# Kernel optimization log

Hardware: AMD Instinct MI355X
Metric: run time of the kernel (lower is better)

Reference implementation:

```python
import jax, jax.numpy as jnp
import numpy as np

NEARZERO = 1e-5
# Parameter bounds in dict order: BETA, FC, K0, K1, K2, LP, PERC, UZL, TT, CFMAX, CFR, CWH
BOUNDS = np.array([[1.0, 6.0], [50.0, 1000.0], [0.05, 0.9], [0.01, 0.5],
                   [0.001, 0.2], [0.2, 1.0], [0.0, 10.0], [0.0, 100.0],
                   [-2.5, 2.5], [0.5, 10.0], [0.0, 0.1], [0.0, 0.2]],
                  dtype=np.float32)


def setup_inputs() -> dict:
    key = jax.random.key(0)
    k1, k2, k3, k4 = jax.random.split(key, 4)
    T, G, nmul = 730, 4000, 8
    prcp = jax.random.uniform(k1, (T, G), dtype=jnp.float32) * 10.0   # mm/day, >= 0
    tmean = jax.random.normal(k2, (T, G), dtype=jnp.float32) * 10.0   # deg C
    pet = jax.random.uniform(k3, (T, G), dtype=jnp.float32) * 5.0     # mm/day, >= 0
    x_hydro_model = jnp.stack([prcp, tmean, pet], axis=-1)            # [T, G, 3]
    params_raw = jax.random.uniform(k4, (1, G, 12, nmul), dtype=jnp.float32)  # in [0,1)
    return {"x_hydro_model": x_hydro_model, "params_raw": params_raw}


def _hbv_forward(x_hydro_model, params_raw):
    G = x_hydro_model.shape[1]
    nmul = params_raw.shape[-1]
    b = jnp.asarray(BOUNDS)
    # change_param_range: param * (ub - lb) + lb, static slice at static_idx=-1
    p = params_raw[-1] * (b[:, 1] - b[:, 0])[None, :, None] + b[:, 0][None, :, None]  # [G,12,nmul]
    (BETA, FC, K0, K1, K2, LP, PERCc, UZL, TT, CFMAX, CFR, CWH) = [p[:, i, :] for i in range(12)]

    Pm = x_hydro_model[:, :, 0][:, :, None]    # [T, G, 1] broadcasts over nmul
    Tm = x_hydro_model[:, :, 1][:, :, None]
    PETm = x_hydro_model[:, :, 2][:, :, None]

    init = jnp.full((G, nmul), 0.001, dtype=jnp.float32)
    carry0 = (init, init, init, init, init)  # SNOWPACK, MELTWATER, SM, SUZ, SLZ

    def step(carry, inputs):
        SNOWPACK, MELTWATER, SM, SUZ, SLZ = carry
        PRECIP, Tt, PETt = inputs  # each [G, 1]
        is_rain = (Tt >= TT).astype(jnp.float32)
        RAIN = PRECIP * is_rain
        SNOW = PRECIP * (1.0 - is_rain)
        SNOWPACK = SNOWPACK + SNOW
        melt = jnp.minimum(jnp.maximum(CFMAX * (Tt - TT), 0.0), SNOWPACK)
        MELTWATER = MELTWATER + melt
        SNOWPACK = SNOWPACK - melt
        refreezing = jnp.minimum(jnp.maximum(CFR * CFMAX * (TT - Tt), 0.0), MELTWATER)
        SNOWPACK = SNOWPACK + refreezing
        MELTWATER = MELTWATER - refreezing
        tosoil = jnp.maximum(MELTWATER - CWH * SNOWPACK, 0.0)
        MELTWATER = MELTWATER - tosoil
        soil_wetness = jnp.clip((SM / FC) ** BETA, 0.0, 1.0)
        recharge = (RAIN + tosoil) * soil_wetness
        SM = SM + RAIN + tosoil - recharge
        excess = jnp.maximum(SM - FC, 0.0)
        SM = SM - excess
        evapfactor = jnp.clip(SM / (LP * FC), 0.0, 1.0)
        ETact = jnp.minimum(SM, PETt * evapfactor)
        SM = jnp.maximum(SM - ETact, NEARZERO)
        SUZ = SUZ + recharge + excess
        PERC = jnp.minimum(SUZ, PERCc)
        SUZ = SUZ - PERC
        Q0 = K0 * jnp.maximum(SUZ - UZL, 0.0)
        SUZ = SUZ - Q0
        Q1 = K1 * SUZ
        SUZ = SUZ - Q1
        SLZ = SLZ + PERC
        Q2 = K2 * SLZ
        SLZ = SLZ - Q2
        return (SNOWPACK, MELTWATER, SM, SUZ, SLZ), Q0 + Q1 + Q2

    _, Qsimmu = jax.lax.scan(step, carry0, (Pm, Tm, PETm))  # [T, G, nmul]
    return Qsimmu


def reference(x_hydro_model, params_raw):
    return _hbv_forward(x_hydro_model, params_raw)
```

## Files before the change

kernel.cpp:

```cpp
#include <hip/hip_runtime.h>
#include <math.h>
#include <stdint.h>

#define NM 8
#define NPAR 12
#define TCH 128
#define CHDW (TCH*24)
#define NLL 12

typedef __attribute__((address_space(1))) const void gv_t;
typedef __attribute__((address_space(3))) void lv_t;

__global__ __launch_bounds__(64, 1) void hbv_kernel(
    const float* __restrict__ x,
    const float* __restrict__ praw,
    float* __restrict__ out,
    int G, int T)
{
    __shared__ float lds[2][CHDW];

    const int lane = threadIdx.x;
    const int b    = blockIdx.x;
    const int g0   = b << 3;
    const int gl   = lane >> 3;
    const int m    = lane & 7;
    const int g    = g0 + gl;

    const float lb[NPAR] = {1.0f, 50.0f, 0.05f, 0.01f, 0.001f, 0.2f, 0.0f, 0.0f, -2.5f, 0.5f, 0.0f, 0.0f};
    const float ub[NPAR] = {6.0f, 1000.0f, 0.9f, 0.5f, 0.2f, 1.0f, 10.0f, 100.0f, 2.5f, 10.0f, 0.1f, 0.2f};

    float p[NPAR];
    const float* pr = praw + (size_t)g * (NPAR * NM) + m;
    #pragma unroll
    for (int i = 0; i < NPAR; ++i) p[i] = pr[i * NM] * (ub[i] - lb[i]) + lb[i];

    const float BETA = p[0], FC = p[1], K0 = p[2], K1 = p[3], K2 = p[4], LP = p[5],
                PERCc = p[6], UZL = p[7], TT = p[8], CFMAX = p[9], CFR = p[10], CWH = p[11];

    const float invLPFC     = 1.0f / (LP * FC);
    const float nCFMAX_TT   = -(CFMAX * TT);
    const float nCFRCFMAX   = -(CFR * CFMAX);
    const float CFRCFMAX_TT = (CFR * CFMAX) * TT;
    const float nBLFC       = -BETA * __builtin_amdgcn_logf(FC);
    const float OMK0        = 1.0f - K0;
    const float K0UZL       = K0 * UZL;
    const float OMK1        = 1.0f - K1;
    const float OMK2        = 1.0f - K2;

    float SP = 0.001f, MW = 0.001f, SM = 0.001f, SUZ = 0.001f, SLZ = 0.001f;

    const char* xb = (const char*)x;
    const uint32_t xstep  = (uint32_t)G * 12u;
    const uint32_t gbase  = (uint32_t)g0 * 12u;
    const uint32_t lin    = (uint32_t)lane * 16u;
    const uint32_t r0     = lin / 96u;
    const uint32_t c0     = lin % 96u;
    const uint32_t rowmax = (uint32_t)(T - 1);

    #define ISSUE_CHUNK(cs_, nb_)                                              \
    {                                                                          \
        uint32_t row_ = (uint32_t)(cs_) + r0;                                  \
        uint32_t col_ = c0;                                                    \
        _Pragma("unroll")                                                      \
        for (int i_ = 0; i_ < NLL; ++i_) {                                     \
            const uint32_t rg_ = row_ < rowmax ? row_ : rowmax;                \
            const uint32_t go_ = rg_ * xstep + gbase + col_;                   \
            __builtin_amdgcn_global_load_lds((gv_t*)(xb + go_),                \
                (lv_t*)&lds[nb_][i_ * 256], 16, 0, 0);                         \
                  \
            row_ += 10u + (col_ >= 32u ? 1u : 0u);                             \
            col_  = (col_ >= 32u) ? (col_ - 32u) : (col_ + 64u);               \
        }                                                                      \
    }

    auto step = [&](float P, float Tt, float E) -> float {
        const float RAIN = (Tt >= TT) ? P : 0.0f;
        const float SNOW = P - RAIN;
        const float mc = fmaxf(fmaf(CFMAX, Tt, nCFMAX_TT), 0.0f);
        const float rc = fmaxf(fmaf(nCFRCFMAX, Tt, CFRCFMAX_TT), 0.0f);
        const float Pe = E * invLPFC;

        SP += SNOW;
        const float melt = fminf(mc, SP);
        MW += melt;
        SP -= melt;
        const float refr = fminf(rc, MW);
        SP += refr;
        MW -= refr;
        const float cw = CWH * SP;
        const float ts = fmaxf(MW - cw, 0.0f);
        MW = fminf(MW, cw);

        const float lg = __builtin_amdgcn_logf(SM);
        const float bl = fminf(fmaf(BETA, lg, nBLFC), 0.0f);
        const float sw = __builtin_amdgcn_exp2f(bl);
        const float rt = RAIN + ts;
        const float rg = rt * sw;
        SM = SM + rt - rg;
        const float ex = fmaxf(SM - FC, 0.0f);
        SM = fminf(SM, FC);
        const float et = fminf(fminf(SM, SM * Pe), E);
        SM = fmaxf(SM - et, 1e-5f);

        SUZ = SUZ + rg + ex;
        const float pc = fminf(SUZ, PERCc);
        const float s2 = fmaxf(SUZ - PERCc, 0.0f);
        const float s3 = fminf(s2, fmaf(OMK0, s2, K0UZL));
        const float s4 = s3 * OMK1;
        SUZ = s4;
        const float sl = SLZ + pc;
        const float q2 = K2 * sl;
        SLZ = sl * OMK2;
        return (s2 - s4) + q2;
    };

    ISSUE_CHUNK(0, 0)

    char* ob = (char*)out;
    uint32_t ooff = (uint32_t)(g * NM + m) * 4u;
    const uint32_t ostep = (uint32_t)(G * NM) * 4u;

    int c = 0;
    for (int cs = 0; cs < T; cs += TCH, ++c) {
        const int nb = c & 1;
        if (cs + TCH < T) {
            ISSUE_CHUNK(cs + TCH, nb ^ 1)
            asm volatile("s_waitcnt vmcnt(12)" ::: "memory");
        } else {
            asm volatile("s_waitcnt vmcnt(0)" ::: "memory");
        }

        const int tcnt = (T - cs < TCH) ? (T - cs) : TCH;
        const float* L = &lds[nb][gl * 3];
        #pragma unroll 8
        for (int tt = 0; tt < tcnt; ++tt) {
            const float P = L[0], Tt = L[1], E = L[2];
            L += 24;
            const float Q = step(P, Tt, E);
            *(float*)(ob + ooff) = Q;
            ooff += ostep;
        }
    }
    #undef ISSUE_CHUNK
}

extern "C" void kernel_launch(void* const* d_in, const int* in_sizes, int n_in,
                              void* d_out, int out_size, void* d_ws, size_t ws_size,
                              hipStream_t stream) {
    const float* x    = (const float*)d_in[0];
    const float* praw = (const float*)d_in[1];
    float* out = (float*)d_out;

    const int G = in_sizes[1] / (NPAR * NM);
    const int T = in_sizes[0] / (3 * G);

    const int grid = G / 8;
    hbv_kernel<<<grid, 64, 0, stream>>>(x, praw, out, G, T);
}
```

Measured before the change: 85.38 us.

## Split HBV recurrence into snow and soil warps pipelined through LDS ring

Each block now runs two wavefronts. One loads the forcing chunks and runs the snow routine, writing rain-plus-meltwater and PET into a double-buffered LDS ring. The second consumes the ring one chunk later and runs the soil and groundwater routines plus output stores. Splitting the serial per-step dependency chain across two waves is meant to shorten the critical path per time step. The cost is a __syncthreads per chunk of 32 steps, extra LDS traffic, and twice the threads per block.

Result: faster. 81.26 us (-4.8%).

```diff
diff --git a/kernel.cpp b/kernel.cpp
--- a/kernel.cpp
+++ b/kernel.cpp
@@ -4,22 +4,23 @@
 
 #define NM 8
 #define NPAR 12
-#define TCH 128
-#define CHDW (TCH*24)
-#define NLL 12
+#define KS 32
+#define NLL 3
 
 typedef __attribute__((address_space(1))) const void gv_t;
 typedef __attribute__((address_space(3))) void lv_t;
 
-__global__ __launch_bounds__(64, 1) void hbv_kernel(
+__global__ __launch_bounds__(128, 1) void hbv_kernel(
     const float* __restrict__ x,
     const float* __restrict__ praw,
     float* __restrict__ out,
     int G, int T)
 {
-    __shared__ float lds[2][CHDW];
+    __shared__ float  fbuf[2][KS * 24];
+    __shared__ float2 ring[2][KS][64];
 
-    const int lane = threadIdx.x;
+    const int wid  = threadIdx.x >> 6;
+    const int lane = threadIdx.x & 63;
     const int b    = blockIdx.x;
     const int g0   = b << 3;
     const int gl   = lane >> 3;
@@ -34,114 +35,135 @@
     #pragma unroll
     for (int i = 0; i < NPAR; ++i) p[i] = pr[i * NM] * (ub[i] - lb[i]) + lb[i];
 
-    const float BETA = p[0], FC = p[1], K0 = p[2], K1 = p[3], K2 = p[4], LP = p[5],
-                PERCc = p[6], UZL = p[7], TT = p[8], CFMAX = p[9], CFR = p[10], CWH = p[11];
+    const int NBLK = (T + KS - 1) / KS;
 
-    const float invLPFC     = 1.0f / (LP * FC);
-    const float nCFMAX_TT   = -(CFMAX * TT);
-    const float nCFRCFMAX   = -(CFR * CFMAX);
-    const float CFRCFMAX_TT = (CFR * CFMAX) * TT;
-    const float nBLFC       = -BETA * __builtin_amdgcn_logf(FC);
-    const float OMK0        = 1.0f - K0;
-    const float K0UZL       = K0 * UZL;
-    const float OMK1        = 1.0f - K1;
-    const float OMK2        = 1.0f - K2;
+    if (wid == 0) {
+        const float TT = p[8], CFMAX = p[9], CFR = p[10], CWH = p[11];
+        const float nCFMAX_TT   = -(CFMAX * TT);
+        const float nCFRCFMAX   = -(CFR * CFMAX);
+        const float CFRCFMAX_TT = (CFR * CFMAX) * TT;
 
-    float SP = 0.001f, MW = 0.001f, SM = 0.001f, SUZ = 0.001f, SLZ = 0.001f;
+        float SP = 0.001f, MW = 0.001f;
 
-    const char* xb = (const char*)x;
-    const uint32_t xstep  = (uint32_t)G * 12u;
-    const uint32_t gbase  = (uint32_t)g0 * 12u;
-    const uint32_t lin    = (uint32_t)lane * 16u;
-    const uint32_t r0     = lin / 96u;
-    const uint32_t c0     = lin % 96u;
-    const uint32_t rowmax = (uint32_t)(T - 1);
+        const char* xb = (const char*)x;
+        const uint32_t xstep  = (uint32_t)G * 12u;
+        const uint32_t gbase  = (uint32_t)g0 * 12u;
+        const uint32_t lin    = (uint32_t)lane * 16u;
+        const uint32_t r0     = lin / 96u;
+        const uint32_t c0     = lin % 96u;
+        const uint32_t rowmax = (uint32_t)(T - 1);
 
-    #define ISSUE_CHUNK(cs_, nb_)                                              \
-    {                                                                          \
-        uint32_t row_ = (uint32_t)(cs_) + r0;                                  \
-        uint32_t col_ = c0;                                                    \
-        _Pragma("unroll")                                                      \
-        for (int i_ = 0; i_ < NLL; ++i_) {                                     \
-            const uint32_t rg_ = row_ < rowmax ? row_ : rowmax;                \
-            const uint32_t go_ = rg_ * xstep + gbase + col_;                   \
-            __builtin_amdgcn_global_load_lds((gv_t*)(xb + go_),                \
-                (lv_t*)&lds[nb_][i_ * 256], 16, 0, 0);                         \
-                  \
-            row_ += 10u + (col_ >= 32u ? 1u : 0u);                             \
-            col_  = (col_ >= 32u) ? (col_ - 32u) : (col_ + 64u);               \
-        }                                                                      \
-    }
-
-    auto step = [&](float P, float Tt, float E) -> float {
-        const float RAIN = (Tt >= TT) ? P : 0.0f;
-        const float SNOW = P - RAIN;
-        const float mc = fmaxf(fmaf(CFMAX, Tt, nCFMAX_TT), 0.0f);
-        const float rc = fmaxf(fmaf(nCFRCFMAX, Tt, CFRCFMAX_TT), 0.0f);
-        const float Pe = E * invLPFC;
-
-        SP += SNOW;
-        const float melt = fminf(mc, SP);
-        MW += melt;
-        SP -= melt;
-        const float refr = fminf(rc, MW);
-        SP += refr;
-        MW -= refr;
-        const float cw = CWH * SP;
-        const float ts = fmaxf(MW - cw, 0.0f);
-        MW = fminf(MW, cw);
-
-        const float lg = __builtin_amdgcn_logf(SM);
-        const float bl = fminf(fmaf(BETA, lg, nBLFC), 0.0f);
-        const float sw = __builtin_amdgcn_exp2f(bl);
-        const float rt = RAIN + ts;
-        const float rg = rt * sw;
-        SM = SM + rt - rg;
-        const float ex = fmaxf(SM - FC, 0.0f);
-        SM = fminf(SM, FC);
-        const float et = fminf(fminf(SM, SM * Pe), E);
-        SM = fmaxf(SM - et, 1e-5f);
-
-        SUZ = SUZ + rg + ex;
-        const float pc = fminf(SUZ, PERCc);
-        const float s2 = fmaxf(SUZ - PERCc, 0.0f);
-        const float s3 = fminf(s2, fmaf(OMK0, s2, K0UZL));
-        const float s4 = s3 * OMK1;
-        SUZ = s4;
-        const float sl = SLZ + pc;
-        const float q2 = K2 * sl;
-        SLZ = sl * OMK2;
-        return (s2 - s4) + q2;
-    };
-
-    ISSUE_CHUNK(0, 0)
-
-    char* ob = (char*)out;
-    uint32_t ooff = (uint32_t)(g * NM + m) * 4u;
-    const uint32_t ostep = (uint32_t)(G * NM) * 4u;
-
-    int c = 0;
-    for (int cs = 0; cs < T; cs += TCH, ++c) {
-        const int nb = c & 1;
-        if (cs + TCH < T) {
-            ISSUE_CHUNK(cs + TCH, nb ^ 1)
-            asm volatile("s_waitcnt vmcnt(12)" ::: "memory");
-        } else {
-            asm volatile("s_waitcnt vmcnt(0)" ::: "memory");
+        #define ISSUE_CHUNK(cs_, nb_)                                          \
+        {                                                                      \
+            uint32_t row_ = (uint32_t)(cs_) + r0;                              \
+            uint32_t col_ = c0;                                                \
+            _Pragma("unroll")                                                  \
+            for (int i_ = 0; i_ < NLL; ++i_) {                                 \
+                const uint32_t rg_ = row_ < rowmax ? row_ : rowmax;            \
+                const uint32_t go_ = rg_ * xstep + gbase + col_;               \
+                __builtin_amdgcn_global_load_lds((gv_t*)(xb + go_),            \
+                    (lv_t*)&fbuf[nb_][i_ * 256], 16, 0, 0);                    \
+                         \
+                row_ += 10u + (col_ >= 32u ? 1u : 0u);                         \
+                col_  = (col_ >= 32u) ? (col_ - 32u) : (col_ + 64u);           \
+            }                                                                  \
         }
 
-        const int tcnt = (T - cs < TCH) ? (T - cs) : TCH;
-        const float* L = &lds[nb][gl * 3];
-        #pragma unroll 8
-        for (int tt = 0; tt < tcnt; ++tt) {
-            const float P = L[0], Tt = L[1], E = L[2];
-            L += 24;
-            const float Q = step(P, Tt, E);
-            *(float*)(ob + ooff) = Q;
-            ooff += ostep;
+        ISSUE_CHUNK(0, 0)
+
+        for (int r = 0; r <= NBLK; ++r) {
+            if (r < NBLK) {
+                if (r + 1 < NBLK) {
+                    ISSUE_CHUNK((r + 1) * KS, (r + 1) & 1)
+                    asm volatile("s_waitcnt vmcnt(3)" ::: "memory");
+                } else {
+                    asm volatile("s_waitcnt vmcnt(0)" ::: "memory");
+                }
+                const int cnt = (T - r * KS < KS) ? (T - r * KS) : KS;
+                const float*  F = &fbuf[r & 1][gl * 3];
+                float2*       R = &ring[r & 1][0][lane];
+                #pragma unroll 4
+                for (int tt = 0; tt < cnt; ++tt) {
+                    const float P = F[0], Tt = F[1], E = F[2];
+                    F += 24;
+                    const float RAIN = (Tt >= TT) ? P : 0.0f;
+                    const float SNOW = P - RAIN;
+                    const float mc = fmaxf(fmaf(CFMAX, Tt, nCFMAX_TT), 0.0f);
+                    const float rc = fmaxf(fmaf(nCFRCFMAX, Tt, CFRCFMAX_TT), 0.0f);
+                    SP += SNOW;
+                    const float melt = fminf(mc, SP);
+                    MW += melt;
+                    SP -= melt;
+                    const float refr = fminf(rc, MW);
+                    SP += refr;
+                    MW -= refr;
+                    const float cw = CWH * SP;
+                    const float ts = fmaxf(MW - cw, 0.0f);
+                    MW = fminf(MW, cw);
+                    float2 rel; rel.x = RAIN + ts; rel.y = E;
+                    *R = rel;
+                    R += 64;
+                }
+            }
+            __syncthreads();
+        }
+        #undef ISSUE_CHUNK
+    } else {
+        const float BETA = p[0], FC = p[1], K0 = p[2], K1 = p[3], K2 = p[4],
+                    LP = p[5], PERCc = p[6], UZL = p[7];
+        const float invLPFC = 1.0f / (LP * FC);
+        const float nBLFC   = -BETA * __builtin_amdgcn_logf(FC);
+        const float OMK0    = 1.0f - K0;
+        const float K0UZL   = K0 * UZL;
+        const float OMK1    = 1.0f - K1;
+        const float OMK2    = 1.0f - K2;
+
+        float SM = 0.001f, SUZ = 0.001f, SLZ = 0.001f;
+
+        char* ob = (char*)out;
+        uint32_t ooff = (uint32_t)(g * NM + m) * 4u;
+        const uint32_t ostep = (uint32_t)(G * NM) * 4u;
+
+        for (int r = 0; r <= NBLK; ++r) {
+            if (r >= 1) {
+                const int base = (r - 1) * KS;
+                const int cnt  = (T - base < KS) ? (T - base) : KS;
+                const float2* R = &ring[(r - 1) & 1][0][lane];
+                #pragma unroll 4
+                for (int tt = 0; tt < cnt; ++tt) {
+                    const float2 rel = *R;
+                    R += 64;
+                    const float rt = rel.x, E = rel.y;
+
+                    const float lg = __builtin_amdgcn_logf(SM);
+                    const float bl = fminf(fmaf(BETA, lg, nBLFC), 0.0f);
+                    const float sw = __builtin_amdgcn_exp2f(bl);
+                    const float rg = rt * sw;
+                    SM = SM + rt - rg;
+                    const float ex = fmaxf(SM - FC, 0.0f);
+                    SM = fminf(SM, FC);
+                    const float Pe = E * invLPFC;
+                    const float et = fminf(fminf(SM, SM * Pe), E);
+                    SM = fmaxf(SM - et, 1e-5f);
+
+                    SUZ = SUZ + rg + ex;
+                    const float pc = fminf(SUZ, PERCc);
+                    const float s2 = fmaxf(SUZ - PERCc, 0.0f);
+                    const float s3 = fminf(s2, fmaf(OMK0, s2, K0UZL));
+                    const float s4 = s3 * OMK1;
+                    SUZ = s4;
+                    const float sl = SLZ + pc;
+                    const float q2 = K2 * sl;
+                    SLZ = sl * OMK2;
+                    const float Q = (s2 - s4) + q2;
+
+                    *(float*)(ob + ooff) = Q;
+                    ooff += ostep;
+                }
+            }
+            __syncthreads();
         }
     }
-    #undef ISSUE_CHUNK
 }
 
 extern "C" void kernel_launch(void* const* d_in, const int* in_sizes, int n_in,
@@ -155,5 +177,5 @@
     const int T = in_sizes[0] / (3 * G);
 
     const int grid = G / 8;
-    hbv_kernel<<<grid, 64, 0, stream>>>(x, praw, out, G, T);
+    hbv_kernel<<<grid, 128, 0, stream>>>(x, praw, out, G, T);
 }
```

## Process two ensemble members per thread with packed fp16 soil and routing states

Applied to the files above, without the earlier changes.

Each thread now integrates two nmul members, so a block covers 16 grid cells and the grid is halved. The LDS chunk layout and the async load pattern are resized to match. Soil moisture is rewritten as a deficit from field capacity, and the soil and upper-zone routing updates run as packed half-precision pairs, while snow and the lower zone stay in fp32; outputs are stored as float2. The aim is more independent work per thread to hide the serial recurrence latency, plus fewer ALU instructions. The cost is that long-horizon state accumulated in fp16 may drift from the fp32 reference.

Result: slower. 136.3 us (+59.6%).

```diff
diff --git a/kernel.cpp b/kernel.cpp
--- a/kernel.cpp
+++ b/kernel.cpp
@@ -4,12 +4,22 @@
 
 #define NM 8
 #define NPAR 12
+#define GPB 16
 #define TCH 128
-#define CHDW (TCH*24)
-#define NLL 12
+#define ROWDW (GPB*3)
+#define CHDW (TCH*ROWDW)
+#define NLL  (CHDW*4/1024)
 
 typedef __attribute__((address_space(1))) const void gv_t;
 typedef __attribute__((address_space(3))) void lv_t;
+typedef float v2f __attribute__((ext_vector_type(2)));
+typedef _Float16 h2 __attribute__((ext_vector_type(2)));
+
+static __device__ __forceinline__ h2 h2min(h2 a, h2 b) { return __builtin_elementwise_min(a, b); }
+static __device__ __forceinline__ h2 h2max(h2 a, h2 b) { return __builtin_elementwise_max(a, b); }
+static __device__ __forceinline__ h2 mkh2(float a, float b) {
+    h2 r; r.x = (_Float16)a; r.y = (_Float16)b; return r;
+}
 
 __global__ __launch_bounds__(64, 1) void hbv_kernel(
     const float* __restrict__ x,
@@ -21,40 +31,55 @@
 
     const int lane = threadIdx.x;
     const int b    = blockIdx.x;
-    const int g0   = b << 3;
-    const int gl   = lane >> 3;
-    const int m    = lane & 7;
-    const int g    = g0 + gl;
+    const int gl   = lane >> 2;
+    const int pi   = lane & 3;
+    const int g    = (b << 4) + gl;
+    const int m0   = pi << 1;
 
     const float lb[NPAR] = {1.0f, 50.0f, 0.05f, 0.01f, 0.001f, 0.2f, 0.0f, 0.0f, -2.5f, 0.5f, 0.0f, 0.0f};
     const float ub[NPAR] = {6.0f, 1000.0f, 0.9f, 0.5f, 0.2f, 1.0f, 10.0f, 100.0f, 2.5f, 10.0f, 0.1f, 0.2f};
 
-    float p[NPAR];
-    const float* pr = praw + (size_t)g * (NPAR * NM) + m;
+    float pA[NPAR], pB[NPAR];
+    const float* pr = praw + (size_t)g * (NPAR * NM) + m0;
     #pragma unroll
-    for (int i = 0; i < NPAR; ++i) p[i] = pr[i * NM] * (ub[i] - lb[i]) + lb[i];
-
-    const float BETA = p[0], FC = p[1], K0 = p[2], K1 = p[3], K2 = p[4], LP = p[5],
-                PERCc = p[6], UZL = p[7], TT = p[8], CFMAX = p[9], CFR = p[10], CWH = p[11];
-
-    const float invLPFC     = 1.0f / (LP * FC);
-    const float nCFMAX_TT   = -(CFMAX * TT);
-    const float nCFRCFMAX   = -(CFR * CFMAX);
-    const float CFRCFMAX_TT = (CFR * CFMAX) * TT;
-    const float nBLFC       = -BETA * __builtin_amdgcn_logf(FC);
-    const float OMK0        = 1.0f - K0;
-    const float K0UZL       = K0 * UZL;
-    const float OMK1        = 1.0f - K1;
-    const float OMK2        = 1.0f - K2;
-
-    float SP = 0.001f, MW = 0.001f, SM = 0.001f, SUZ = 0.001f, SLZ = 0.001f;
+    for (int i = 0; i < NPAR; ++i) {
+        const float s = ub[i] - lb[i];
+        pA[i] = pr[i * NM]     * s + lb[i];
+        pB[i] = pr[i * NM + 1] * s + lb[i];
+    }
+
+    const float TTa = pA[8],  TTb = pB[8];
+    const float CFa = pA[9],  CFb = pB[9];
+    const float nCMTTa = -(CFa * TTa),         nCMTTb = -(CFb * TTb);
+    const float nCRa   = -(pA[10] * CFa),      nCRb   = -(pB[10] * CFb);
+    const float CRTTa  = (pA[10] * CFa) * TTa, CRTTb  = (pB[10] * CFb) * TTb;
+    const float CWa = pA[11], CWb = pB[11];
+    const float FCa = pA[1],  FCb = pB[1];
+    const float iLPa = 1.0f / (pA[5] * FCa),   iLPb = 1.0f / (pB[5] * FCb);
+    const float BEa = pA[0], BEb = pB[0];
+    const float nBLa = -BEa * __builtin_amdgcn_logf(FCa);
+    const float nBLb = -BEb * __builtin_amdgcn_logf(FCb);
+    const float K2a = pA[4], K2b = pB[4];
+    const float OK2a = 1.0f - K2a, OK2b = 1.0f - K2b;
+
+    const h2 FC2  = mkh2(FCa, FCb);
+    const h2 PC2  = mkh2(pA[6], pB[6]);
+    const h2 UZL2 = mkh2(pA[7], pB[7]);
+    const h2 K0h  = mkh2(pA[2], pB[2]);
+    const h2 K1h  = mkh2(pA[3], pB[3]);
+    const h2 Z2   = mkh2(0.0f, 0.0f);
+
+    float SPa = 0.001f, SPb = 0.001f, MWa = 0.001f, MWb = 0.001f;
+    float SLZa = 0.001f, SLZb = 0.001f;
+    h2 D   = mkh2(FCa - 0.001f, FCb - 0.001f);
+    h2 SUZ = mkh2(0.001f, 0.001f);
 
     const char* xb = (const char*)x;
     const uint32_t xstep  = (uint32_t)G * 12u;
-    const uint32_t gbase  = (uint32_t)g0 * 12u;
+    const uint32_t gbase  = (uint32_t)(b << 4) * 12u;
     const uint32_t lin    = (uint32_t)lane * 16u;
-    const uint32_t r0     = lin / 96u;
-    const uint32_t c0     = lin % 96u;
+    const uint32_t r0     = lin / 192u;
+    const uint32_t c0     = lin % 192u;
     const uint32_t rowmax = (uint32_t)(T - 1);
 
     #define ISSUE_CHUNK(cs_, nb_)                                              \
@@ -67,57 +92,74 @@
             const uint32_t go_ = rg_ * xstep + gbase + col_;                   \
             __builtin_amdgcn_global_load_lds((gv_t*)(xb + go_),                \
                 (lv_t*)&lds[nb_][i_ * 256], 16, 0, 0);                         \
-                  \
-            row_ += 10u + (col_ >= 32u ? 1u : 0u);                             \
-            col_  = (col_ >= 32u) ? (col_ - 32u) : (col_ + 64u);               \
+            row_ += 5u + (col_ >= 128u ? 1u : 0u);                             \
+            col_  = (col_ >= 128u) ? (col_ - 128u) : (col_ + 64u);             \
         }                                                                      \
     }
 
-    auto step = [&](float P, float Tt, float E) -> float {
-        const float RAIN = (Tt >= TT) ? P : 0.0f;
-        const float SNOW = P - RAIN;
-        const float mc = fmaxf(fmaf(CFMAX, Tt, nCFMAX_TT), 0.0f);
-        const float rc = fmaxf(fmaf(nCFRCFMAX, Tt, CFRCFMAX_TT), 0.0f);
-        const float Pe = E * invLPFC;
-
-        SP += SNOW;
-        const float melt = fminf(mc, SP);
-        MW += melt;
-        SP -= melt;
-        const float refr = fminf(rc, MW);
-        SP += refr;
-        MW -= refr;
-        const float cw = CWH * SP;
-        const float ts = fmaxf(MW - cw, 0.0f);
-        MW = fminf(MW, cw);
-
-        const float lg = __builtin_amdgcn_logf(SM);
-        const float bl = fminf(fmaf(BETA, lg, nBLFC), 0.0f);
-        const float sw = __builtin_amdgcn_exp2f(bl);
-        const float rt = RAIN + ts;
-        const float rg = rt * sw;
-        SM = SM + rt - rg;
-        const float ex = fmaxf(SM - FC, 0.0f);
-        SM = fminf(SM, FC);
-        const float et = fminf(fminf(SM, SM * Pe), E);
-        SM = fmaxf(SM - et, 1e-5f);
-
-        SUZ = SUZ + rg + ex;
-        const float pc = fminf(SUZ, PERCc);
-        const float s2 = fmaxf(SUZ - PERCc, 0.0f);
-        const float s3 = fminf(s2, fmaf(OMK0, s2, K0UZL));
-        const float s4 = s3 * OMK1;
-        SUZ = s4;
-        const float sl = SLZ + pc;
-        const float q2 = K2 * sl;
-        SLZ = sl * OMK2;
-        return (s2 - s4) + q2;
+    auto step = [&](float P, float Tt, float E) -> v2f {
+        const float rainA = (Tt >= TTa) ? P : 0.0f;
+        const float rainB = (Tt >= TTb) ? P : 0.0f;
+        const float snowA = P - rainA,  snowB = P - rainB;
+        const float mcA = fmaxf(fmaf(CFa, Tt, nCMTTa), 0.0f);
+        const float mcB = fmaxf(fmaf(CFb, Tt, nCMTTb), 0.0f);
+        const float rcA = fmaxf(fmaf(nCRa, Tt, CRTTa), 0.0f);
+        const float rcB = fmaxf(fmaf(nCRb, Tt, CRTTb), 0.0f);
+
+        SPa += snowA;                             SPb += snowB;
+        const float meltA = fminf(mcA, SPa);      const float meltB = fminf(mcB, SPb);
+        MWa += meltA;                             MWb += meltB;
+        SPa -= meltA;                             SPb -= meltB;
+        const float refA = fminf(rcA, MWa);       const float refB = fminf(rcB, MWb);
+        SPa += refA;                              SPb += refB;
+        MWa -= refA;                              MWb -= refB;
+        const float cwA = CWa * SPa;              const float cwB = CWb * SPb;
+        const float tsA = fmaxf(MWa - cwA, 0.0f); const float tsB = fmaxf(MWb - cwB, 0.0f);
+        MWa = fminf(MWa, cwA);                    MWb = fminf(MWb, cwB);
+
+        const float smA = fmaxf(FCa - (float)D.x, 0.0f);
+        const float smB = fmaxf(FCb - (float)D.y, 0.0f);
+        const float swA = __builtin_amdgcn_exp2f(
+            fminf(fmaf(BEa, __builtin_amdgcn_logf(smA), nBLa), 0.0f));
+        const float swB = __builtin_amdgcn_exp2f(
+            fminf(fmaf(BEb, __builtin_amdgcn_logf(smB), nBLb), 0.0f));
+        const float rtA = rainA + tsA;            const float rtB = rainB + tsB;
+        const float rgA = rtA * swA;              const float rgB = rtB * swB;
+
+        const h2 tmr = mkh2(rtA - rgA, rtB - rgB);
+        const h2 Pe2 = mkh2(E * iLPa, E * iLPb);
+        const h2 Eh  = mkh2(E, E);
+        const h2 D1  = D - tmr;
+        const h2 ex  = h2max(Z2 - D1, Z2);
+        const h2 D2  = h2max(D1, Z2);
+        const h2 SM2 = FC2 - D2;
+        const h2 et  = h2min(h2min(SM2, SM2 * Pe2), Eh);
+        D = h2min(D2 + et, FC2);
+
+        const h2 rg2 = mkh2(rgA, rgB);
+        SUZ = SUZ + (rg2 + ex);
+        const h2 pc = h2min(SUZ, PC2);
+        SUZ = SUZ - pc;
+        const h2 q0 = K0h * h2max(SUZ - UZL2, Z2);
+        SUZ = SUZ - q0;
+        const h2 q1 = K1h * SUZ;
+        SUZ = SUZ - q1;
+        const h2 q01 = q0 + q1;
+
+        const float slA = SLZa + (float)pc.x;
+        const float slB = SLZb + (float)pc.y;
+        const float q2A = K2a * slA;
+        const float q2B = K2b * slB;
+        SLZa = slA * OK2a;
+        SLZb = slB * OK2b;
+        v2f q; q.x = (float)q01.x + q2A; q.y = (float)q01.y + q2B;
+        return q;
     };
 
     ISSUE_CHUNK(0, 0)
 
     char* ob = (char*)out;
-    uint32_t ooff = (uint32_t)(g * NM + m) * 4u;
+    uint32_t ooff = (uint32_t)(g * NM + m0) * 4u;
     const uint32_t ostep = (uint32_t)(G * NM) * 4u;
 
     int c = 0;
@@ -125,7 +167,7 @@
         const int nb = c & 1;
         if (cs + TCH < T) {
             ISSUE_CHUNK(cs + TCH, nb ^ 1)
-            asm volatile("s_waitcnt vmcnt(12)" ::: "memory");
+            asm volatile("s_waitcnt vmcnt(24)" ::: "memory");
         } else {
             asm volatile("s_waitcnt vmcnt(0)" ::: "memory");
         }
@@ -135,9 +177,9 @@
         #pragma unroll 8
         for (int tt = 0; tt < tcnt; ++tt) {
             const float P = L[0], Tt = L[1], E = L[2];
-            L += 24;
-            const float Q = step(P, Tt, E);
-            *(float*)(ob + ooff) = Q;
+            L += ROWDW;
+            const v2f q = step(P, Tt, E);
+            *(v2f*)(ob + ooff) = q;
             ooff += ostep;
         }
     }
@@ -154,6 +196,6 @@
     const int G = in_sizes[1] / (NPAR * NM);
     const int T = in_sizes[0] / (3 * G);
 
-    const int grid = G / 8;
+    const int grid = G / GPB;
     hbv_kernel<<<grid, 64, 0, stream>>>(x, praw, out, G, T);
 }
```
